# Optimization experiments

Hardware: AMD Instinct MI355X
Metric: run time of the kernel (lower is better)

Reference implementation:

```python
import jax, jax.numpy as jnp
import numpy as np
import math

D_MODEL = 1024
N_HEADS = 16
D_K = 64
CHUNK_LEN = 64


def setup_inputs() -> dict:
    key = jax.random.key(0)
    ks = jax.random.split(key, 12)
    hd = N_HEADS * D_K
    s = 0.02
    return {
        'h': jax.random.normal(ks[0], (4, 2048, D_MODEL), jnp.float32),
        'e': jax.random.normal(ks[1], (4, 32, 2, 128, D_MODEL), jnp.float32),
        'Wq': jax.random.normal(ks[2], (D_MODEL, hd), jnp.float32) * s,
        'bq': jnp.zeros((hd,), jnp.float32),
        'Wk': jax.random.normal(ks[3], (D_MODEL, hd), jnp.float32) * s,
        'bk': jnp.zeros((hd,), jnp.float32),
        'Wv': jax.random.normal(ks[4], (D_MODEL, hd), jnp.float32) * s,
        'bv': jnp.zeros((hd,), jnp.float32),
        'Wo': jax.random.normal(ks[5], (hd, D_MODEL), jnp.float32) * s,
        'bo': jnp.zeros((D_MODEL,), jnp.float32),
        'gamma': jnp.ones((D_MODEL,), jnp.float32),
        'beta': jnp.zeros((D_MODEL,), jnp.float32),
    }


def reference(h, e, Wq, bq, Wk, bk, Wv, bv, Wo, bo, gamma, beta):
    b, chunks, neighbors, nlen, d_model = e.shape
    seq_len = h.shape[1]
    scale = 1.0 / math.sqrt(D_K)
    h_res = h
    # shift so chunk i attends to neighbors retrieved for chunk i
    hh = h[:, CHUNK_LEN - 1:]
    # layer norm
    mu = jnp.mean(hh, axis=-1, keepdims=True)
    var = jnp.mean(jnp.square(hh - mu), axis=-1, keepdims=True)
    hh = (hh - mu) / jnp.sqrt(var + 1e-5) * gamma + beta
    # pad to chunks * CHUNK_LEN
    pad = chunks * CHUNK_LEN - hh.shape[1]
    hh = jnp.pad(hh, ((0, 0), (0, pad), (0, 0)))
    hh = hh.reshape(b, chunks, CHUNK_LEN, d_model)
    q = (hh @ Wq + bq).reshape(b, chunks, CHUNK_LEN, N_HEADS, D_K)
    k = (e @ Wk + bk).reshape(b, chunks, neighbors, nlen, N_HEADS, D_K)
    v = (e @ Wv + bv).reshape(b, chunks, neighbors, nlen, N_HEADS, D_K)
    attn = jnp.einsum('bcihd,bcnjhd->bchinj', q, k) * scale  # [b,c,h,i,n,j]
    a_shape = attn.shape
    attn = jax.nn.softmax(attn.reshape(*a_shape[:-2], -1), axis=-1).reshape(a_shape)
    out = jnp.einsum('bchinj,bcnjhd->bcihd', attn, v)
    out = out.reshape(b, chunks * CHUNK_LEN, N_HEADS * D_K)
    out = out @ Wo + bo
    out = jnp.pad(out, ((0, 0), (CHUNK_LEN - 1, 0), (0, 0)))
    return out[:, :seq_len] + h_res
```

## Files before the change

kernel.cpp:

```cpp
#include <hip/hip_runtime.h>
#include <cstdint>
#include <cstddef>


typedef float f32x4 __attribute__((ext_vector_type(4)));
typedef __bf16 bf16x8 __attribute__((ext_vector_type(8)));

static __device__ __forceinline__ ushort f2bf(float f) {
  union { float f; uint32_t u; } x; x.f = f;
  uint32_t r = x.u + 0x7fffu + ((x.u >> 16) & 1u);
  return (ushort)(r >> 16);
}

static __device__ __forceinline__ bf16x8 ld_frag(const ushort* p) {
  union { uint4 u; bf16x8 v; } x;
  x.u = *(const uint4*)p;
  return x.v;
}

static __device__ __forceinline__ void gl2lds16(const ushort* g, ushort* l) {
  __builtin_amdgcn_global_load_lds(
      (const __attribute__((address_space(1))) void*)g,
      (__attribute__((address_space(3))) void*)l,
      16, 0, 0);
}

__global__ __launch_bounds__(256) void transpose_cast(const float* __restrict__ W,
                                                      ushort* __restrict__ WT) {
  __shared__ float tile[64][65];
  const int t = threadIdx.x;
  const int n0 = blockIdx.x * 64, k0 = blockIdx.y * 64;
#pragma unroll
  for (int i = 0; i < 4; ++i) {
    int lid = i * 256 + t;
    int r = lid >> 4, c4 = (lid & 15) * 4;
    float4 v = *(const float4*)&W[(size_t)(k0 + r) * 1024 + n0 + c4];
    tile[r][c4 + 0] = v.x; tile[r][c4 + 1] = v.y;
    tile[r][c4 + 2] = v.z; tile[r][c4 + 3] = v.w;
  }
  __syncthreads();
#pragma unroll
  for (int i = 0; i < 4; ++i) {
    int lid = i * 256 + t;
    int n = lid >> 4, k4 = (lid & 15) * 4;
    ushort4 o;
    o.x = f2bf(tile[k4 + 0][n]); o.y = f2bf(tile[k4 + 1][n]);
    o.z = f2bf(tile[k4 + 2][n]); o.w = f2bf(tile[k4 + 3][n]);
    *(ushort4*)&WT[(size_t)(n0 + n) * 1024 + k0 + k4] = o;
  }
}

__global__ __launch_bounds__(256) void cast_bf16(const float* __restrict__ x,
                                                 ushort* __restrict__ y) {
  const size_t i = ((size_t)blockIdx.x * 256 + threadIdx.x) * 8;
  float4 a = *(const float4*)&x[i];
  float4 b = *(const float4*)&x[i + 4];
  ushort o[8];
  o[0] = f2bf(a.x); o[1] = f2bf(a.y); o[2] = f2bf(a.z); o[3] = f2bf(a.w);
  o[4] = f2bf(b.x); o[5] = f2bf(b.y); o[6] = f2bf(b.z); o[7] = f2bf(b.w);
  *(uint4*)&y[i] = *(const uint4*)o;
}

__global__ __launch_bounds__(256) void ln_kernel(const float* __restrict__ h,
                                                 const float* __restrict__ gamma,
                                                 const float* __restrict__ beta,
                                                 ushort* __restrict__ hh) {
  const int bx = blockIdx.x;
  const int b = bx >> 11, s = bx & 2047;
  const int t = threadIdx.x;
  ushort* orow = hh + (size_t)(b * 2048 + s) * 1024;
  if (s >= 1985) {
    ushort4 z; z.x = 0; z.y = 0; z.z = 0; z.w = 0;
    *(ushort4*)&orow[t * 4] = z;
    return;
  }
  const float* xrow = h + (size_t)(b * 2048 + 63 + s) * 1024;
  float4 x = *(const float4*)&xrow[t * 4];
  float s1 = x.x + x.y + x.z + x.w;
  float s2 = x.x * x.x + x.y * x.y + x.z * x.z + x.w * x.w;
#pragma unroll
  for (int off = 32; off > 0; off >>= 1) {
    s1 += __shfl_xor(s1, off);
    s2 += __shfl_xor(s2, off);
  }
  __shared__ float a1[4], a2[4];
  if ((t & 63) == 0) { a1[t >> 6] = s1; a2[t >> 6] = s2; }
  __syncthreads();
  s1 = a1[0] + a1[1] + a1[2] + a1[3];
  s2 = a2[0] + a2[1] + a2[2] + a2[3];
  const float mu = s1 * (1.0f / 1024.0f);
  const float var = s2 * (1.0f / 1024.0f) - mu * mu;
  const float rstd = rsqrtf(var + 1e-5f);
  float4 g = *(const float4*)&gamma[t * 4];
  float4 be = *(const float4*)&beta[t * 4];
  ushort4 o;
  o.x = f2bf((x.x - mu) * rstd * g.x + be.x);
  o.y = f2bf((x.y - mu) * rstd * g.y + be.y);
  o.z = f2bf((x.z - mu) * rstd * g.z + be.z);
  o.w = f2bf((x.w - mu) * rstd * g.w + be.w);
  *(ushort4*)&orow[t * 4] = o;
}

template <int MODE>
__global__ __launch_bounds__(256) void gemm_bf16(const ushort* __restrict__ A,
                                                 const ushort* __restrict__ Bt,
                                                 const float* __restrict__ bias,
                                                 ushort* __restrict__ Cbf,
                                                 float* __restrict__ Cf,
                                                 const float* __restrict__ resid,
                                                 int mtiles, int mrow_off) {
  __shared__ __align__(16) ushort Alds[128 * 32];
  __shared__ __align__(16) ushort Blds[128 * 32];
  const int t = threadIdx.x;
  const int lane = t & 63, wave = t >> 6;
  const int quad = lane >> 4, l16 = lane & 15;

  const int L = blockIdx.x;
  const int xcd = L & 7, slot = L >> 3;
  const int mt = xcd * (mtiles >> 3) + (slot >> 3);
  const int nt = slot & 7;
  const int m0 = mt * 128, n0 = nt * 128;

  const int srow = lane >> 2;
  const int scol = (lane & 3) * 8;
  const int c0 = wave * 2;
  const ushort* gA0 = A  + (size_t)(m0 + c0 * 16 + srow) * 1024 + scol;
  const ushort* gA1 = gA0 + 16 * 1024;
  const ushort* gB0 = Bt + (size_t)(n0 + c0 * 16 + srow) * 1024 + scol;
  const ushort* gB1 = gB0 + 16 * 1024;
  ushort* dA0 = &Alds[c0 * 512 + lane * 8];
  ushort* dA1 = dA0 + 512;
  ushort* dB0 = &Blds[c0 * 512 + lane * 8];
  ushort* dB1 = dB0 + 512;

  const int wrow = (wave >> 1) * 64, wcol = (wave & 1) * 64;
  const ushort* pA = &Alds[(wrow + l16) * 32 + quad * 8];
  const ushort* pB = &Blds[(wcol + l16) * 32 + quad * 8];

  f32x4 zero = {0.f, 0.f, 0.f, 0.f};
  f32x4 acc[4][4];
#pragma unroll
  for (int i = 0; i < 4; ++i)
#pragma unroll
    for (int j = 0; j < 4; ++j) acc[i][j] = zero;

  for (int kb = 0; kb < 32; ++kb) {
    const int ko = kb * 32;
    gl2lds16(gA0 + ko, dA0);
    gl2lds16(gA1 + ko, dA1);
    gl2lds16(gB0 + ko, dB0);
    gl2lds16(gB1 + ko, dB1);
    __syncthreads();
    bf16x8 af[4], bfv[4];
#pragma unroll
    for (int i = 0; i < 4; ++i) af[i]  = ld_frag(pA + i * 16 * 32);
#pragma unroll
    for (int j = 0; j < 4; ++j) bfv[j] = ld_frag(pB + j * 16 * 32);
#pragma unroll
    for (int i = 0; i < 4; ++i)
#pragma unroll
      for (int j = 0; j < 4; ++j)
        acc[i][j] = __builtin_amdgcn_mfma_f32_16x16x32_bf16(af[i], bfv[j], acc[i][j], 0, 0, 0);
    __syncthreads();
  }

#pragma unroll
  for (int mi = 0; mi < 4; ++mi)
#pragma unroll
    for (int mj = 0; mj < 4; ++mj) {
      const int cc = n0 + wcol + mj * 16 + l16;
      const float bv = bias[cc];
#pragma unroll
      for (int rr = 0; rr < 4; ++rr) {
        const int r = m0 + wrow + mi * 16 + quad * 4 + rr;
        const float val = acc[mi][mj][rr] + bv;
        if constexpr (MODE == 0) {
          Cbf[(size_t)r * 1024 + cc] = f2bf(val);
        } else {
          const int gr = r + mrow_off;
          const int b = gr >> 11, s = gr & 2047;
          if (s < 1985) {
            const size_t o = (size_t)(b * 2048 + s + 63) * 1024 + cc;
            Cf[o] = val + resid[o];
          }
        }
      }
    }
}

__global__ __launch_bounds__(256) void attn_kernel(const ushort* __restrict__ Qb,
                                                   const ushort* __restrict__ Kb,
                                                   const ushort* __restrict__ Vb,
                                                   ushort* __restrict__ Ob) {
  __shared__ __align__(16) ushort smem[4608 + 18432 + 16896];
  __shared__ float redm[4][64];
  __shared__ float reds[4][64];
  ushort* Qs = smem;
  ushort* Ks = smem + 4608;
  ushort* Vt = smem + 23040;
  ushort* Ps = smem;

  const int t = threadIdx.x;
  const int bx = blockIdx.x;
  const int hd = bx & 15, c = (bx >> 4) & 31, b = bx >> 9;
  const int lane = t & 63, wave = t >> 6;
  const int quad = lane >> 4, l16 = lane & 15;

  const int qrow0 = b * 2048 + c * 64;
  const int kvrow0 = (b * 32 + c) * 256;
  const int colh = hd * 64;

#pragma unroll
  for (int it = 0; it < 2; ++it) {
    int lid = it * 256 + t;
    int r = lid >> 3, ch = (lid & 7) * 8;
    uint4 v = *(const uint4*)&Qb[(size_t)(qrow0 + r) * 1024 + colh + ch];
    *(uint4*)&Qs[r * 72 + ch] = v;
  }
#pragma unroll
  for (int it = 0; it < 8; ++it) {
    int lid = it * 256 + t;
    int r = lid >> 3, ch = (lid & 7) * 8;
    uint4 v = *(const uint4*)&Kb[(size_t)(kvrow0 + r) * 1024 + colh + ch];
    *(uint4*)&Ks[r * 72 + ch] = v;
  }
#pragma unroll
  for (int it = 0; it < 8; ++it) {
    int lid = it * 256 + t;
    int r = lid >> 3, ch = (lid & 7) * 8;
    uint4 v = *(const uint4*)&Vb[(size_t)(kvrow0 + r) * 1024 + colh + ch];
    uint32_t u0 = v.x, u1 = v.y, u2 = v.z, u3 = v.w;
    Vt[(ch + 0) * 264 + r] = (ushort)(u0 & 0xffff);
    Vt[(ch + 1) * 264 + r] = (ushort)(u0 >> 16);
    Vt[(ch + 2) * 264 + r] = (ushort)(u1 & 0xffff);
    Vt[(ch + 3) * 264 + r] = (ushort)(u1 >> 16);
    Vt[(ch + 4) * 264 + r] = (ushort)(u2 & 0xffff);
    Vt[(ch + 5) * 264 + r] = (ushort)(u2 >> 16);
    Vt[(ch + 6) * 264 + r] = (ushort)(u3 & 0xffff);
    Vt[(ch + 7) * 264 + r] = (ushort)(u3 >> 16);
  }
  __syncthreads();

  const int jw = wave * 64;
  f32x4 zero = {0.f, 0.f, 0.f, 0.f};
  f32x4 acc[4][4];
#pragma unroll
  for (int i = 0; i < 4; ++i)
#pragma unroll
    for (int j = 0; j < 4; ++j) acc[i][j] = zero;

#pragma unroll
  for (int kb = 0; kb < 2; ++kb) {
    bf16x8 af[4], bfv[4];
#pragma unroll
    for (int mi = 0; mi < 4; ++mi)
      af[mi] = ld_frag(&Qs[(mi * 16 + l16) * 72 + kb * 32 + quad * 8]);
#pragma unroll
    for (int mj = 0; mj < 4; ++mj)
      bfv[mj] = ld_frag(&Ks[(jw + mj * 16 + l16) * 72 + kb * 32 + quad * 8]);
#pragma unroll
    for (int mi = 0; mi < 4; ++mi)
#pragma unroll
      for (int mj = 0; mj < 4; ++mj)
        acc[mi][mj] = __builtin_amdgcn_mfma_f32_16x16x32_bf16(af[mi], bfv[mj], acc[mi][mj], 0, 0, 0);
  }
#pragma unroll
  for (int mi = 0; mi < 4; ++mi)
#pragma unroll
    for (int mj = 0; mj < 4; ++mj) acc[mi][mj] = acc[mi][mj] * 0.125f;

  float rmax[4][4];
#pragma unroll
  for (int mi = 0; mi < 4; ++mi)
#pragma unroll
    for (int rr = 0; rr < 4; ++rr) {
      float m = fmaxf(fmaxf(acc[mi][0][rr], acc[mi][1][rr]),
                      fmaxf(acc[mi][2][rr], acc[mi][3][rr]));
      m = fmaxf(m, __shfl_xor(m, 1));
      m = fmaxf(m, __shfl_xor(m, 2));
      m = fmaxf(m, __shfl_xor(m, 4));
      m = fmaxf(m, __shfl_xor(m, 8));
      rmax[mi][rr] = m;
    }
  if (l16 == 0) {
#pragma unroll
    for (int mi = 0; mi < 4; ++mi)
#pragma unroll
      for (int rr = 0; rr < 4; ++rr)
        redm[wave][mi * 16 + quad * 4 + rr] = rmax[mi][rr];
  }
  __syncthreads();
  float gmax[4][4];
#pragma unroll
  for (int mi = 0; mi < 4; ++mi)
#pragma unroll
    for (int rr = 0; rr < 4; ++rr) {
      const int row = mi * 16 + quad * 4 + rr;
      gmax[mi][rr] = fmaxf(fmaxf(redm[0][row], redm[1][row]),
                           fmaxf(redm[2][row], redm[3][row]));
    }
  float rsum[4][4];
#pragma unroll
  for (int mi = 0; mi < 4; ++mi)
#pragma unroll
    for (int rr = 0; rr < 4; ++rr) {
      float s = 0.f;
#pragma unroll
      for (int mj = 0; mj < 4; ++mj) {
        float p = exp2f((acc[mi][mj][rr] - gmax[mi][rr]) * 1.4426950408889634f);
        acc[mi][mj][rr] = p;
        s += p;
      }
      s += __shfl_xor(s, 1);
      s += __shfl_xor(s, 2);
      s += __shfl_xor(s, 4);
      s += __shfl_xor(s, 8);
      rsum[mi][rr] = s;
    }
  if (l16 == 0) {
#pragma unroll
    for (int mi = 0; mi < 4; ++mi)
#pragma unroll
      for (int rr = 0; rr < 4; ++rr)
        reds[wave][mi * 16 + quad * 4 + rr] = rsum[mi][rr];
  }
  __syncthreads();
#pragma unroll
  for (int mi = 0; mi < 4; ++mi)
#pragma unroll
    for (int rr = 0; rr < 4; ++rr) {
      const int row = mi * 16 + quad * 4 + rr;
      const float inv = 1.0f / (reds[0][row] + reds[1][row] + reds[2][row] + reds[3][row]);
#pragma unroll
      for (int mj = 0; mj < 4; ++mj)
        Ps[row * 264 + jw + mj * 16 + l16] = f2bf(acc[mi][mj][rr] * inv);
    }
  __syncthreads();

  const int d0 = wave * 16;
  f32x4 acc2[4];
#pragma unroll
  for (int mi = 0; mi < 4; ++mi) acc2[mi] = zero;
#pragma unroll
  for (int kb = 0; kb < 8; ++kb) {
    bf16x8 bfv = ld_frag(&Vt[(d0 + l16) * 264 + kb * 32 + quad * 8]);
#pragma unroll
    for (int mi = 0; mi < 4; ++mi) {
      bf16x8 af = ld_frag(&Ps[(mi * 16 + l16) * 264 + kb * 32 + quad * 8]);
      acc2[mi] = __builtin_amdgcn_mfma_f32_16x16x32_bf16(af, bfv, acc2[mi], 0, 0, 0);
    }
  }
#pragma unroll
  for (int mi = 0; mi < 4; ++mi)
#pragma unroll
    for (int rr = 0; rr < 4; ++rr) {
      const int i = mi * 16 + quad * 4 + rr;
      Ob[(size_t)(qrow0 + i) * 1024 + colh + d0 + l16] = f2bf(acc2[mi][rr]);
    }
}

__global__ __launch_bounds__(256) void head_copy(const float* __restrict__ h,
                                                 float* __restrict__ out) {
  const int idx4 = blockIdx.x * 256 + threadIdx.x;
  const int b = idx4 / 16128;
  const int rem = idx4 - b * 16128;
  const size_t o = (size_t)b * 2048 * 1024 + (size_t)rem * 4;
  *(float4*)&out[o] = *(const float4*)&h[o];
}

extern "C" void kernel_launch(void* const* d_in, const int* in_sizes, int n_in,
                              void* d_out, int out_size, void* d_ws, size_t ws_size,
                              hipStream_t stream) {
  const float* h     = (const float*)d_in[0];
  const float* e     = (const float*)d_in[1];
  const float* Wq    = (const float*)d_in[2];
  const float* bq    = (const float*)d_in[3];
  const float* Wk    = (const float*)d_in[4];
  const float* bk    = (const float*)d_in[5];
  const float* Wv    = (const float*)d_in[6];
  const float* bv    = (const float*)d_in[7];
  const float* Wo    = (const float*)d_in[8];
  const float* bo    = (const float*)d_in[9];
  const float* gamma = (const float*)d_in[10];
  const float* beta  = (const float*)d_in[11];
  float* out = (float*)d_out;

  char* ws = (char*)d_ws;
  ushort* WqT = (ushort*)(ws + ((size_t)0 << 20));
  ushort* WkT = (ushort*)(ws + ((size_t)2 << 20));
  ushort* WvT = (ushort*)(ws + ((size_t)4 << 20));
  ushort* WoT = (ushort*)(ws + ((size_t)6 << 20));
  ushort* hhb = (ushort*)(ws + ((size_t)8 << 20));
  ushort* Qb  = (ushort*)(ws + ((size_t)24 << 20));
  ushort* Kb  = (ushort*)(ws + ((size_t)40 << 20));
  ushort* Vb  = (ushort*)(ws + ((size_t)104 << 20));
  ushort* Ob  = (ushort*)(ws + ((size_t)168 << 20));

  transpose_cast<<<dim3(16, 16), 256, 0, stream>>>(Wq, WqT);
  transpose_cast<<<dim3(16, 16), 256, 0, stream>>>(Wk, WkT);
  transpose_cast<<<dim3(16, 16), 256, 0, stream>>>(Wv, WvT);
  transpose_cast<<<dim3(16, 16), 256, 0, stream>>>(Wo, WoT);

  ln_kernel<<<8192, 256, 0, stream>>>(h, gamma, beta, hhb);

  gemm_bf16<0><<<512, 256, 0, stream>>>(hhb, WqT, bq, Qb, nullptr, nullptr, 64, 0);

  for (int q = 0; q < 4; ++q) {
    const size_t roff = (size_t)q * 8192 * 1024;
    cast_bf16<<<4096, 256, 0, stream>>>(e + roff, hhb);
    gemm_bf16<0><<<512, 256, 0, stream>>>(hhb, WkT, bk, Kb + roff, nullptr, nullptr, 64, 0);
    gemm_bf16<0><<<512, 256, 0, stream>>>(hhb, WvT, bv, Vb + roff, nullptr, nullptr, 64, 0);
  }

  attn_kernel<<<2048, 256, 0, stream>>>(Qb, Kb, Vb, Ob);

  gemm_bf16<1><<<512, 256, 0, stream>>>(Ob, WoT, bo, nullptr, out, h, 64, 0);
  head_copy<<<252, 256, 0, stream>>>(h, out);
}
```

Before: 609.5 us.

## Fuse K/V projections into one GEMM writing transposed V; fold scale into Q

Merges the four weight transpose launches into one 3D-grid launch. Concatenates Wk and Wv so each e-chunk needs one GEMM with 16 N-tiles instead of two launches, re-reading the A tile once. The V half of the epilogue writes V directly in a per-(batch,chunk,head) transposed layout so the attention kernel can copy it with vector loads instead of doing a scalar LDS transpose. The softmax scale is folded into the Q projection epilogue, removing the multiply in attention. Risk: the transposed V stores are 8-byte scattered writes, which may coalesce poorly.

Result: no change. 605.6 us (-0.6%).

```diff
diff --git a/kernel.cpp b/kernel.cpp
--- a/kernel.cpp
+++ b/kernel.cpp
@@ -25,8 +25,20 @@
       16, 0, 0);
 }
 
-__global__ __launch_bounds__(256) void transpose_cast(const float* __restrict__ W,
-                                                      ushort* __restrict__ WT) {
+__global__ __launch_bounds__(256) void transpose_cast4(const float* __restrict__ Wq,
+                                                       const float* __restrict__ Wk,
+                                                       const float* __restrict__ Wv,
+                                                       const float* __restrict__ Wo,
+                                                       ushort* __restrict__ WqT,
+                                                       ushort* __restrict__ WkvT,
+                                                       ushort* __restrict__ WoT) {
+  const float* W; ushort* WT;
+  switch (blockIdx.z) {
+    case 0:  W = Wq; WT = WqT; break;
+    case 1:  W = Wk; WT = WkvT; break;
+    case 2:  W = Wv; WT = WkvT + (size_t)1024 * 1024; break;
+    default: W = Wo; WT = WoT; break;
+  }
   __shared__ float tile[64][65];
   const int t = threadIdx.x;
   const int n0 = blockIdx.x * 64, k0 = blockIdx.y * 64;
@@ -101,14 +113,16 @@
   *(ushort4*)&orow[t * 4] = o;
 }
 
-template <int MODE>
+template <int MODE, int NT>
 __global__ __launch_bounds__(256) void gemm_bf16(const ushort* __restrict__ A,
                                                  const ushort* __restrict__ Bt,
                                                  const float* __restrict__ bias,
+                                                 const float* __restrict__ bias2,
                                                  ushort* __restrict__ Cbf,
+                                                 ushort* __restrict__ Vtg,
                                                  float* __restrict__ Cf,
                                                  const float* __restrict__ resid,
-                                                 int mtiles, int mrow_off) {
+                                                 int mtiles, float scale) {
   __shared__ __align__(16) ushort Alds[128 * 32];
   __shared__ __align__(16) ushort Blds[128 * 32];
   const int t = threadIdx.x;
@@ -117,8 +131,8 @@
 
   const int L = blockIdx.x;
   const int xcd = L & 7, slot = L >> 3;
-  const int mt = xcd * (mtiles >> 3) + (slot >> 3);
-  const int nt = slot & 7;
+  const int nt = slot & (NT - 1);
+  const int mt = xcd * (mtiles >> 3) + (slot / NT);
   const int m0 = mt * 128, n0 = nt * 128;
 
   const int srow = lane >> 2;
@@ -169,19 +183,39 @@
 #pragma unroll
     for (int mj = 0; mj < 4; ++mj) {
       const int cc = n0 + wcol + mj * 16 + l16;
-      const float bv = bias[cc];
-#pragma unroll
-      for (int rr = 0; rr < 4; ++rr) {
-        const int r = m0 + wrow + mi * 16 + quad * 4 + rr;
-        const float val = acc[mi][mj][rr] + bv;
-        if constexpr (MODE == 0) {
-          Cbf[(size_t)r * 1024 + cc] = f2bf(val);
+      const int r0 = m0 + wrow + mi * 16 + quad * 4;
+      if constexpr (MODE == 0) {
+        const float bvb = bias[cc];
+#pragma unroll
+        for (int rr = 0; rr < 4; ++rr)
+          Cbf[(size_t)(r0 + rr) * 1024 + cc] = f2bf((acc[mi][mj][rr] + bvb) * scale);
+      } else if constexpr (MODE == 2) {
+        if (nt < 8) {
+          const float bvb = bias[cc];
+#pragma unroll
+          for (int rr = 0; rr < 4; ++rr)
+            Cbf[(size_t)(r0 + rr) * 1024 + cc] = f2bf(acc[mi][mj][rr] + bvb);
         } else {
-          const int gr = r + mrow_off;
-          const int b = gr >> 11, s = gr & 2047;
+          const int cv = cc - 1024;
+          const int hh_ = cv >> 6, dd = cv & 63;
+          const float bvb = bias2[cv];
+          const int bcl = r0 >> 8, j0 = r0 & 255;
+          ushort4 o;
+          o.x = f2bf(acc[mi][mj][0] + bvb);
+          o.y = f2bf(acc[mi][mj][1] + bvb);
+          o.z = f2bf(acc[mi][mj][2] + bvb);
+          o.w = f2bf(acc[mi][mj][3] + bvb);
+          *(ushort4*)&Vtg[((size_t)(bcl * 16 + hh_)) * 16384 + dd * 256 + j0] = o;
+        }
+      } else {
+        const float bvb = bias[cc];
+#pragma unroll
+        for (int rr = 0; rr < 4; ++rr) {
+          const int r = r0 + rr;
+          const int b = r >> 11, s = r & 2047;
           if (s < 1985) {
             const size_t o = (size_t)(b * 2048 + s + 63) * 1024 + cc;
-            Cf[o] = val + resid[o];
+            Cf[o] = acc[mi][mj][rr] + bvb + resid[o];
           }
         }
       }
@@ -190,7 +224,7 @@
 
 __global__ __launch_bounds__(256) void attn_kernel(const ushort* __restrict__ Qb,
                                                    const ushort* __restrict__ Kb,
-                                                   const ushort* __restrict__ Vb,
+                                                   const ushort* __restrict__ Vtg,
                                                    ushort* __restrict__ Ob) {
   __shared__ __align__(16) ushort smem[4608 + 18432 + 16896];
   __shared__ float redm[4][64];
@@ -209,6 +243,7 @@
   const int qrow0 = b * 2048 + c * 64;
   const int kvrow0 = (b * 32 + c) * 256;
   const int colh = hd * 64;
+  const ushort* vsrc = Vtg + ((size_t)((b * 32 + c) * 16 + hd)) * 16384;
 
 #pragma unroll
   for (int it = 0; it < 2; ++it) {
@@ -227,17 +262,9 @@
 #pragma unroll
   for (int it = 0; it < 8; ++it) {
     int lid = it * 256 + t;
-    int r = lid >> 3, ch = (lid & 7) * 8;
-    uint4 v = *(const uint4*)&Vb[(size_t)(kvrow0 + r) * 1024 + colh + ch];
-    uint32_t u0 = v.x, u1 = v.y, u2 = v.z, u3 = v.w;
-    Vt[(ch + 0) * 264 + r] = (ushort)(u0 & 0xffff);
-    Vt[(ch + 1) * 264 + r] = (ushort)(u0 >> 16);
-    Vt[(ch + 2) * 264 + r] = (ushort)(u1 & 0xffff);
-    Vt[(ch + 3) * 264 + r] = (ushort)(u1 >> 16);
-    Vt[(ch + 4) * 264 + r] = (ushort)(u2 & 0xffff);
-    Vt[(ch + 5) * 264 + r] = (ushort)(u2 >> 16);
-    Vt[(ch + 6) * 264 + r] = (ushort)(u3 & 0xffff);
-    Vt[(ch + 7) * 264 + r] = (ushort)(u3 >> 16);
+    int row = lid >> 5, c8 = (lid & 31) * 8;
+    uint4 v = *(const uint4*)&vsrc[row * 256 + c8];
+    *(uint4*)&Vt[row * 264 + c8] = v;
   }
   __syncthreads();
 
@@ -264,10 +291,6 @@
       for (int mj = 0; mj < 4; ++mj)
         acc[mi][mj] = __builtin_amdgcn_mfma_f32_16x16x32_bf16(af[mi], bfv[mj], acc[mi][mj], 0, 0, 0);
   }
-#pragma unroll
-  for (int mi = 0; mi < 4; ++mi)
-#pragma unroll
-    for (int mj = 0; mj < 4; ++mj) acc[mi][mj] = acc[mi][mj] * 0.125f;
 
   float rmax[4][4];
 #pragma unroll
@@ -386,34 +409,32 @@
   float* out = (float*)d_out;
 
   char* ws = (char*)d_ws;
-  ushort* WqT = (ushort*)(ws + ((size_t)0 << 20));
-  ushort* WkT = (ushort*)(ws + ((size_t)2 << 20));
-  ushort* WvT = (ushort*)(ws + ((size_t)4 << 20));
-  ushort* WoT = (ushort*)(ws + ((size_t)6 << 20));
-  ushort* hhb = (ushort*)(ws + ((size_t)8 << 20));
-  ushort* Qb  = (ushort*)(ws + ((size_t)24 << 20));
-  ushort* Kb  = (ushort*)(ws + ((size_t)40 << 20));
-  ushort* Vb  = (ushort*)(ws + ((size_t)104 << 20));
-  ushort* Ob  = (ushort*)(ws + ((size_t)168 << 20));
-
-  transpose_cast<<<dim3(16, 16), 256, 0, stream>>>(Wq, WqT);
-  transpose_cast<<<dim3(16, 16), 256, 0, stream>>>(Wk, WkT);
-  transpose_cast<<<dim3(16, 16), 256, 0, stream>>>(Wv, WvT);
-  transpose_cast<<<dim3(16, 16), 256, 0, stream>>>(Wo, WoT);
+  ushort* WqT  = (ushort*)(ws + ((size_t)0 << 20));
+  ushort* WkvT = (ushort*)(ws + ((size_t)2 << 20));
+  ushort* WoT  = (ushort*)(ws + ((size_t)6 << 20));
+  ushort* hhb  = (ushort*)(ws + ((size_t)8 << 20));
+  ushort* Qb   = (ushort*)(ws + ((size_t)24 << 20));
+  ushort* Kb   = (ushort*)(ws + ((size_t)40 << 20));
+  ushort* VtG  = (ushort*)(ws + ((size_t)104 << 20));
+  ushort* Ob   = (ushort*)(ws + ((size_t)168 << 20));
+
+  transpose_cast4<<<dim3(16, 16, 4), 256, 0, stream>>>(Wq, Wk, Wv, Wo, WqT, WkvT, WoT);
 
   ln_kernel<<<8192, 256, 0, stream>>>(h, gamma, beta, hhb);
 
-  gemm_bf16<0><<<512, 256, 0, stream>>>(hhb, WqT, bq, Qb, nullptr, nullptr, 64, 0);
+  gemm_bf16<0, 8><<<512, 256, 0, stream>>>(hhb, WqT, bq, nullptr, Qb, nullptr,
+                                           nullptr, nullptr, 64, 0.125f);
 
   for (int q = 0; q < 4; ++q) {
     const size_t roff = (size_t)q * 8192 * 1024;
     cast_bf16<<<4096, 256, 0, stream>>>(e + roff, hhb);
-    gemm_bf16<0><<<512, 256, 0, stream>>>(hhb, WkT, bk, Kb + roff, nullptr, nullptr, 64, 0);
-    gemm_bf16<0><<<512, 256, 0, stream>>>(hhb, WvT, bv, Vb + roff, nullptr, nullptr, 64, 0);
-  }
-
-  attn_kernel<<<2048, 256, 0, stream>>>(Qb, Kb, Vb, Ob);
-
-  gemm_bf16<1><<<512, 256, 0, stream>>>(Ob, WoT, bo, nullptr, out, h, 64, 0);
+    gemm_bf16<2, 16><<<1024, 256, 0, stream>>>(hhb, WkvT, bk, bv, Kb + roff,
+                                               VtG + roff, nullptr, nullptr, 64, 1.0f);
+  }
+
+  attn_kernel<<<2048, 256, 0, stream>>>(Qb, Kb, VtG, Ob);
+
+  gemm_bf16<1, 8><<<512, 256, 0, stream>>>(Ob, WoT, bo, nullptr, nullptr, nullptr,
+                                           out, h, 64, 1.0f);
   head_copy<<<252, 256, 0, stream>>>(h, out);
 }
```
